# Performance work log

Measured on AMD Instinct MI355X. Metric: run time of the kernel, lower is better.

Reference implementation:

```python
import jax, jax.numpy as jnp
import numpy as np

N_NODES = 100000
N_EDGES = 1600000
STATE_DIM = 128
HIDDEN_DIM = 128
ACTION_DIM = 16


def gcn_conv(x, edge_index, W, b, n_nodes):
    """PyG-style GCNConv: add self-loops, symmetric normalization, x@W then aggregate."""
    xw = x @ W  # [N, H]
    loops = jnp.arange(n_nodes, dtype=edge_index.dtype)
    src = jnp.concatenate([edge_index[0], loops])  # [E+N]
    dst = jnp.concatenate([edge_index[1], loops])
    ones = jnp.ones(src.shape[0], dtype=xw.dtype)
    deg = jax.ops.segment_sum(ones, dst, num_segments=n_nodes)  # degree of target nodes
    dinv = jnp.where(deg > 0, jax.lax.rsqrt(deg), 0.0)
    norm = dinv[src] * dinv[dst]  # [E+N]
    msg = xw[src] * norm[:, None]  # gather + scale (irregular access)
    out = jax.ops.segment_sum(msg, dst, num_segments=n_nodes)  # scatter-aggregate
    return out + b


def setup_inputs() -> dict:
    key = jax.random.key(0)
    ks = jax.random.split(key, 12)
    def lin(k, fan_in, shape):
        bound = 1.0 / np.sqrt(fan_in)
        return jax.random.uniform(k, shape, jnp.float32, -bound, bound)
    return {
        "x": jax.random.normal(ks[0], (N_NODES, STATE_DIM), jnp.float32),
        "edge_index": jax.random.randint(ks[1], (2, N_EDGES), 0, N_NODES, jnp.int64),
        "action": jax.random.normal(ks[2], (N_NODES, ACTION_DIM), jnp.float32),
        "gcn1_w": lin(ks[3], STATE_DIM, (STATE_DIM, HIDDEN_DIM)),
        "gcn1_b": lin(ks[4], STATE_DIM, (HIDDEN_DIM,)),
        "gcn2_w": lin(ks[5], HIDDEN_DIM, (HIDDEN_DIM, HIDDEN_DIM)),
        "gcn2_b": lin(ks[6], HIDDEN_DIM, (HIDDEN_DIM,)),
        "fc1_w": lin(ks[7], HIDDEN_DIM + ACTION_DIM, (HIDDEN_DIM + ACTION_DIM, HIDDEN_DIM)),
        "fc1_b": lin(ks[8], HIDDEN_DIM + ACTION_DIM, (HIDDEN_DIM,)),
        "fc2_w": lin(ks[9], HIDDEN_DIM, (HIDDEN_DIM, 1)),
        "fc2_b": lin(ks[10], HIDDEN_DIM, (1,)),
    }


def reference(x, edge_index, action, gcn1_w, gcn1_b, gcn2_w, gcn2_b, fc1_w, fc1_b, fc2_w, fc2_b):
    n = x.shape[0]
    h = jax.nn.relu(gcn_conv(x, edge_index, gcn1_w, gcn1_b, n))
    h = jax.nn.relu(gcn_conv(h, edge_index, gcn2_w, gcn2_b, n))
    h = jnp.concatenate([h, action], axis=-1)  # [N, H+A]
    h = jax.nn.relu(h @ fc1_w + fc1_b)
    q = h @ fc2_w + fc2_b  # [N, 1]
    return q.squeeze(-1)
```

## Files before the change

### kernel.cpp

```cpp
#include <hip/hip_runtime.h>
#include <hip/hip_bf16.h>

typedef unsigned short u16;
typedef unsigned int   u32;
typedef __attribute__((ext_vector_type(8))) short bf16x8;
typedef __attribute__((ext_vector_type(4))) float f32x4;

constexpr int NN = 100000;
constexpr int NE = 1600000;
constexpr int D  = 128;
constexpr size_t WS_NEED = 58909184;

constexpr int NBUCK = 196;
constexpr int NBLKA = 256;
constexpr int EPB   = 6272;
constexpr int CAPA  = 80;

__device__ __forceinline__ float bf2f(u16 u){ union{u32 i;float f;}v; v.i=((u32)u)<<16; return v.f; }
__device__ __forceinline__ float2 bfp(u32 u){ union{u32 i;float f;}a,b; a.i=u<<16; b.i=u&0xffff0000u; return make_float2(a.f,b.f); }
__device__ __forceinline__ u16 f2bf(float f){ union{float f;u32 i;}v; v.f=f; u32 r=v.i + 0x7fffu + ((v.i>>16)&1u); return (u16)(r>>16); }
__device__ __forceinline__ u32 pk2(float a, float b){ return (u32)f2bf(a) | ((u32)f2bf(b)<<16); }

__global__ void detect_kernel(const u32* __restrict__ xw, const int* __restrict__ ei,
                              int* __restrict__ flagf, int* __restrict__ flage){
  __shared__ int shf[256];
  __shared__ int she[256];
  int t = threadIdx.x;
  int cnt = 0;
  for(int i = 0; i < 16; i++){
    u32 w = xw[(t*16 + i) * 256];
    int e = (int)((w >> 7) & 0xFFu);
    cnt += (e >= 64 && e <= 160) ? 1 : 0;
  }
  int nz = 0;
  for(int i = 0; i < 8; i++){
    int k = t*8 + i;
    long long w = 1 + ((long long)k * (2LL*NE - 2)) / 2048;
    nz += (ei[(int)(w | 1)] != 0) ? 1 : 0;
  }
  shf[t] = cnt; she[t] = nz;
  __syncthreads();
  for(int off=128; off>0; off>>=1){
    if(t<off){ shf[t]+=shf[t+off]; she[t]+=she[t+off]; }
    __syncthreads();
  }
  if(t==0){ flagf[0] = (shf[0] < 3000) ? 1 : 0; flage[0] = (she[0] == 0) ? 1 : 0; }
}

__global__ void prep_kernel(const void* __restrict__ w1, const void* __restrict__ w2,
    const void* __restrict__ fw1, const void* __restrict__ b1, const void* __restrict__ b2,
    const void* __restrict__ fb1, const void* __restrict__ fw2, const void* __restrict__ fb2,
    const int* __restrict__ flagf,
    u16* __restrict__ WT1, u16* __restrict__ WT2, u16* __restrict__ WTF, float* __restrict__ BF)
{
  const int ff = flagf[0];
  int i = blockIdx.x*256 + threadIdx.x;
  auto cv = [&](const void* p, int idx)->float{
    return ff ? ((const float*)p)[idx] : bf2f(((const u16*)p)[idx]);
  };
  if(i < 16384){
    int k = i >> 7, d = i & 127;
    WT1[d*128 + k] = f2bf(cv(w1, i));
  }else if(i < 32768){
    int j = i - 16384; int k = j >> 7, d = j & 127;
    WT2[d*128 + k] = f2bf(cv(w2, j));
  }else if(i < 51200){
    int j = i - 32768; int k = j >> 7, d = j & 127;
    WTF[d*144 + k] = f2bf(cv(fw1, j));
  }else if(i < 51713){
    int j = i - 51200;
    if(j < 128)       BF[j]   = cv(b1, j);
    else if(j < 256)  BF[j]   = cv(b2, j-128);
    else if(j < 384)  BF[j]   = cv(fb1, j-256);
    else if(j < 512)  BF[j]   = cv(fw2, j-384);
    else              BF[512] = cv(fb2, 0);
  }
}

__global__ void fill1_kernel(u16* __restrict__ out, int n){
  int i = blockIdx.x*blockDim.x + threadIdx.x;
  if(i < n) out[i] = 0x3F80;
}

__global__ __launch_bounds__(256) void passA_kernel(
    const int* __restrict__ ei, const int* __restrict__ flage,
    u32* __restrict__ ebuf, u32* __restrict__ counts)
{
  __shared__ u32 hist[NBUCK];
  int t = threadIdx.x;
  for(int b = t; b < NBUCK; b += 256) hist[b] = 0;
  __syncthreads();
  const int f = flage[0];
  const int eb = blockIdx.x * EPB;
  const u32 cbase = blockIdx.x * NBUCK;
  for(int i = t; i < EPB; i += 256){
    int e = eb + i;
    if(e >= NE) break;
    int s = f ? ei[2*e]      : ei[e];
    int d = f ? ei[2*(NE+e)] : ei[NE+e];
    if((u32)s >= (u32)NN || (u32)d >= (u32)NN) continue;
    int b = d >> 9;
    u32 rank = atomicAdd(&hist[b], 1u);
    if(rank < CAPA) ebuf[(size_t)(cbase + b)*CAPA + rank] = (u32)s | ((u32)(d & 511) << 17);
  }
  __syncthreads();
  for(int b = t; b < NBUCK; b += 256){
    u32 c = hist[b];
    counts[cbase + b] = (c < CAPA) ? c : CAPA;
  }
}

__global__ void scan196_kernel(const u32* __restrict__ counts, int* __restrict__ bases){
  __shared__ int sh[NBUCK];
  int t = threadIdx.x;
  if(t < NBUCK){
    int tot = 0;
    for(int c = 0; c < NBLKA; c++) tot += counts[c*NBUCK + t];
    sh[t] = tot;
  }
  __syncthreads();
  if(t == 0){
    int acc = 0;
    for(int b = 0; b < NBUCK; b++){ int v = sh[b]; sh[b] = acc; acc += v; }
  }
  __syncthreads();
  if(t < NBUCK) bases[t] = sh[t];
}

__global__ __launch_bounds__(512) void passB_kernel(
    const u32* __restrict__ ebuf, const u32* __restrict__ counts, const int* __restrict__ bases,
    int* __restrict__ deg, int* __restrict__ off, float* __restrict__ dinv,
    int* __restrict__ srcs)
{
  __shared__ int cnt[512];
  __shared__ int nodeoff[512];
  __shared__ int pos[512];
  __shared__ int choff[NBLKA + 1];
  const int t = threadIdx.x;
  const int b = blockIdx.x;
  const int v0 = b << 9;

  cnt[t] = 0;
  __syncthreads();

  if(t < NBLKA) choff[t] = (int)counts[t*NBUCK + b];
  __syncthreads();
  if(t == 0){
    int acc = 0;
    for(int c = 0; c < NBLKA; c++){ int v = choff[c]; choff[c] = acc; acc += v; }
    choff[NBLKA] = acc;
  }
  __syncthreads();
  const int T = choff[NBLKA];

  for(int i = t; i < T; i += 512){
    int lo = 0, hi = NBLKA - 1;
    #pragma unroll
    for(int s = 0; s < 8; s++){
      int mid = (lo + hi) >> 1;
      if(choff[mid + 1] <= i) lo = mid + 1; else hi = mid;
    }
    u32 rec = ebuf[(size_t)(lo*NBUCK + b)*CAPA + (i - choff[lo])];
    atomicAdd(&cnt[rec >> 17], 1);
  }
  __syncthreads();

  int myc = cnt[t];
  nodeoff[t] = myc;
  __syncthreads();
  for(int o = 1; o < 512; o <<= 1){
    int a = (t >= o) ? nodeoff[t - o] : 0;
    __syncthreads();
    nodeoff[t] += a;
    __syncthreads();
  }
  int excl = nodeoff[t] - myc;
  __syncthreads();
  nodeoff[t] = excl;
  pos[t] = 0;
  __syncthreads();

  const int gb = bases[b];

  for(int i = t; i < T; i += 512){
    int lo = 0, hi = NBLKA - 1;
    #pragma unroll
    for(int s = 0; s < 8; s++){
      int mid = (lo + hi) >> 1;
      if(choff[mid + 1] <= i) lo = mid + 1; else hi = mid;
    }
    u32 rec = ebuf[(size_t)(lo*NBUCK + b)*CAPA + (i - choff[lo])];
    int ld = rec >> 17;
    int r = atomicAdd(&pos[ld], 1);
    srcs[gb + nodeoff[ld] + r] = (int)(rec & 0x1FFFFu);
  }

  int v = v0 + t;
  if(v < NN){
    deg[v] = myc;
    off[v] = gb + excl;
    dinv[v] = rsqrtf((float)(myc + 1));
  }
}

template<int K, bool FUSE_Q, bool RAW1, bool RAW2>
__global__ __launch_bounds__(256) void gemm_mfma(
    const void* __restrict__ A1, const void* __restrict__ A2,
    const u16* __restrict__ WT, const float* __restrict__ biasf,
    const float* __restrict__ qwf, const float* __restrict__ qbf,
    const int* __restrict__ flagf, void* __restrict__ out, int n)
{
  constexpr int KT = ((K + 31)/32)*32;
  constexpr int KP = KT + 8;
  __shared__ u16 Ws[128*KP];
  __shared__ u16 As[64*KP];
  const int tid = threadIdx.x;
  const int nb  = blockIdx.x * 64;
  const int ff  = flagf[0];

  constexpr int CPT = KT/8;
  for(int i = tid; i < 128*CPT; i += 256){
    int row = i / CPT, col = (i % CPT) * 8;
    uint4 v = make_uint4(0,0,0,0);
    if(col < K) v = *(const uint4*)(WT + row*K + col);
    *(uint4*)(Ws + row*KP + col) = v;
  }
  for(int i = tid; i < 64*CPT; i += 256){
    int row = i / CPT, col = (i % CPT) * 8;
    int gr = nb + row; if(gr >= n) gr = n-1;
    uint4 v = make_uint4(0,0,0,0);
    if(col < 128){
      if(!RAW1 || !ff){
        v = *(const uint4*)((const u16*)A1 + (size_t)gr*128 + col);
      }else{
        const float* af = (const float*)A1 + (size_t)gr*128 + col;
        float4 p0 = *(const float4*)(af);
        float4 p1 = *(const float4*)(af + 4);
        v.x = pk2(p0.x,p0.y); v.y = pk2(p0.z,p0.w);
        v.z = pk2(p1.x,p1.y); v.w = pk2(p1.z,p1.w);
      }
    }else if(col < K){
      if(!RAW2 || !ff){
        v = *(const uint4*)((const u16*)A2 + (size_t)gr*16 + (col - 128));
      }else{
        const float* af = (const float*)A2 + (size_t)gr*16 + (col - 128);
        float4 p0 = *(const float4*)(af);
        float4 p1 = *(const float4*)(af + 4);
        v.x = pk2(p0.x,p0.y); v.y = pk2(p0.z,p0.w);
        v.z = pk2(p1.x,p1.y); v.w = pk2(p1.z,p1.w);
      }
    }
    *(uint4*)(As + row*KP + col) = v;
  }
  __syncthreads();

  const int wave = tid >> 6;
  const int lane = tid & 63;
  const int quad = lane >> 4;
  const int lm   = lane & 15;

  const u16* Ab = As + (wave*16 + lm)*KP;
  const u16* Bb = Ws + lm*KP;

  f32x4 acc[8];
  #pragma unroll
  for(int t=0;t<8;t++) acc[t] = (f32x4){0.f,0.f,0.f,0.f};

  #pragma unroll
  for(int ki = 0; ki < KT/32; ki++){
    int kk = ki*32 + quad*8;
    bf16x8 a = *(const bf16x8*)(Ab + kk);
    #pragma unroll
    for(int t=0;t<8;t++){
      bf16x8 b = *(const bf16x8*)(Bb + t*16*KP + kk);
      acc[t] = __builtin_amdgcn_mfma_f32_16x16x32_bf16(a, b, acc[t], 0, 0, 0);
    }
  }

  const int node0 = nb + wave*16 + quad*4;
  if(!FUSE_Q){
    #pragma unroll
    for(int t=0;t<8;t++){
      #pragma unroll
      for(int r=0;r<4;r++){
        int gr = node0 + r;
        if(gr < n) ((u16*)out)[(size_t)gr*D + t*16 + lm] = f2bf(acc[t][r]);
      }
    }
  }else{
    float qp[4] = {0.f,0.f,0.f,0.f};
    #pragma unroll
    for(int t=0;t<8;t++){
      float bvt = biasf[t*16 + lm];
      float qwt = qwf[t*16 + lm];
      #pragma unroll
      for(int r=0;r<4;r++){
        float h = fmaxf(acc[t][r] + bvt, 0.f);
        qp[r] += h * qwt;
      }
    }
    #pragma unroll
    for(int r=0;r<4;r++){
      #pragma unroll
      for(int o=1; o<16; o<<=1) qp[r] += __shfl_xor(qp[r], o, 16);
    }
    if(lm == 0){
      float qb = qbf[0];
      #pragma unroll
      for(int r=0;r<4;r++){
        int gr = node0 + r;
        if(gr < n){
          float q = qp[r] + qb;
          if(ff) ((float*)out)[gr] = q;
          else   ((u16*)out)[gr]  = f2bf(q);
        }
      }
    }
  }
}

__global__ __launch_bounds__(256) void gather_kernel(
    const int* __restrict__ off, const int* __restrict__ deg,
    const int* __restrict__ srcs, const float* __restrict__ dinv,
    const u16* __restrict__ xw, const float* __restrict__ biasf,
    u16* __restrict__ h)
{
  int node = blockIdx.x*8 + (threadIdx.x >> 5);
  int lane = threadIdx.x & 31;
  if(node >= NN) return;
  int j0 = off[node];
  int j1 = j0 + deg[node];

  float a0=0.f, a1=0.f, a2=0.f, a3=0.f;
  const size_t lo = 4*lane;
  int j = j0;
  for(; j+4 <= j1; j += 4){
    int s0=srcs[j], s1=srcs[j+1], s2=srcs[j+2], s3=srcs[j+3];
    if((u32)s0>=(u32)NN) s0=node; if((u32)s1>=(u32)NN) s1=node;
    if((u32)s2>=(u32)NN) s2=node; if((u32)s3>=(u32)NN) s3=node;
    float w0=dinv[s0], w1=dinv[s1], w2=dinv[s2], w3=dinv[s3];
    uint2 p0 = *(const uint2*)(xw + (size_t)s0*D + lo);
    uint2 p1 = *(const uint2*)(xw + (size_t)s1*D + lo);
    uint2 p2 = *(const uint2*)(xw + (size_t)s2*D + lo);
    uint2 p3 = *(const uint2*)(xw + (size_t)s3*D + lo);
    float2 f0a=bfp(p0.x), f0b=bfp(p0.y);
    float2 f1a=bfp(p1.x), f1b=bfp(p1.y);
    float2 f2a=bfp(p2.x), f2b=bfp(p2.y);
    float2 f3a=bfp(p3.x), f3b=bfp(p3.y);
    a0 += w0*f0a.x + w1*f1a.x + w2*f2a.x + w3*f3a.x;
    a1 += w0*f0a.y + w1*f1a.y + w2*f2a.y + w3*f3a.y;
    a2 += w0*f0b.x + w1*f1b.x + w2*f2b.x + w3*f3b.x;
    a3 += w0*f0b.y + w1*f1b.y + w2*f2b.y + w3*f3b.y;
  }
  for(; j < j1; j++){
    int s = srcs[j];
    if((u32)s >= (u32)NN) continue;
    float w = dinv[s];
    uint2 p = *(const uint2*)(xw + (size_t)s*D + lo);
    float2 fa=bfp(p.x), fb=bfp(p.y);
    a0 += w*fa.x; a1 += w*fa.y; a2 += w*fb.x; a3 += w*fb.y;
  }

  float dv = dinv[node];
  float dv2 = dv*dv;
  uint2 ps = *(const uint2*)(xw + (size_t)node*D + lo);
  float2 sa=bfp(ps.x), sb=bfp(ps.y);
  float4 bf4 = *(const float4*)(biasf + lo);
  float o0 = fmaxf(dv*a0 + dv2*sa.x + bf4.x, 0.f);
  float o1 = fmaxf(dv*a1 + dv2*sa.y + bf4.y, 0.f);
  float o2 = fmaxf(dv*a2 + dv2*sb.x + bf4.z, 0.f);
  float o3 = fmaxf(dv*a3 + dv2*sb.y + bf4.w, 0.f);
  uint2 pkd; pkd.x = pk2(o0,o1); pkd.y = pk2(o2,o3);
  *(uint2*)(h + (size_t)node*D + lo) = pkd;
}

extern "C" void kernel_launch(void* const* d_in, const int* in_sizes, int n_in,
                              void* d_out, int out_size, void* d_ws, size_t ws_size,
                              hipStream_t stream)
{
  bool meta_ok = (n_in >= 11) && (in_sizes[0] == NN*D) && (in_sizes[1] == 2*NE)
              && (in_sizes[2] == NN*16) && (out_size == NN);
  if(!meta_ok){
    fill1_kernel<<<(NN+255)/256, 256, 0, stream>>>((u16*)d_out, NN);
    return;
  }
  if(ws_size < WS_NEED) return;

  const void* x      = d_in[0];
  const int*  ei     = (const int*)d_in[1];
  const void* action = d_in[2];
  const void* w1     = d_in[3];
  const void* b1     = d_in[4];
  const void* w2     = d_in[5];
  const void* b2     = d_in[6];
  const void* fw1    = d_in[7];
  const void* fb1    = d_in[8];
  const void* fw2    = d_in[9];
  const void* fb2    = d_in[10];

  char* ws = (char*)d_ws;
  int*   DEG    = (int*)(ws + 0);
  int*   OFF    = (int*)(ws + 400128);
  float* DINV   = (float*)(ws + 800256);
  int*   FLAGE  = (int*)(ws + 1204480);
  int*   FLAGF  = (int*)(ws + 1204544);
  u16*   WT1    = (u16*)(ws + 1204608);
  u16*   WT2    = (u16*)(ws + 1237376);
  u16*   WTF    = (u16*)(ws + 1270144);
  float* BF     = (float*)(ws + 1307008);
  int*   SRCS   = (int*)(ws + 1309184);
  u16*   F0     = (u16*)(ws + 7709184);
  u16*   F1     = (u16*)(ws + 33309184);
  u32*   EBUF   = (u32*)(ws + 33309184);
  u32*   COUNTS = (u32*)(ws + 49365504);
  int*   BASES  = (int*)(ws + 49566208);

  detect_kernel<<<1, 256, 0, stream>>>((const u32*)x, ei, FLAGF, FLAGE);

  passA_kernel<<<NBLKA, 256, 0, stream>>>(ei, FLAGE, EBUF, COUNTS);
  scan196_kernel<<<1, 256, 0, stream>>>(COUNTS, BASES);
  passB_kernel<<<NBUCK, 512, 0, stream>>>(EBUF, COUNTS, BASES, DEG, OFF, DINV, SRCS);

  prep_kernel<<<203, 256, 0, stream>>>(w1, w2, fw1, b1, b2, fb1, fw2, fb2, FLAGF,
                                       WT1, WT2, WTF, BF);

  gemm_mfma<128,false,true,false><<<(NN+63)/64, 256, 0, stream>>>(x, nullptr, WT1, nullptr, nullptr, nullptr, FLAGF, F0, NN);
  gather_kernel<<<(NN+7)/8, 256, 0, stream>>>(OFF, DEG, SRCS, DINV, F0, BF, F1);

  gemm_mfma<128,false,false,false><<<(NN+63)/64, 256, 0, stream>>>(F1, nullptr, WT2, nullptr, nullptr, nullptr, FLAGF, F0, NN);
  gather_kernel<<<(NN+7)/8, 256, 0, stream>>>(OFF, DEG, SRCS, DINV, F0, BF+128, F1);

  gemm_mfma<144,true,false,true><<<(NN+63)/64, 256, 0, stream>>>(F1, action, WTF, BF+256, BF+384, BF+512, FLAGF, d_out, NN);
}
```

Before: 369.8 us.

## Fuse neighbor gather into following GEMM kernels, removing intermediate round-trips

The gather-aggregate step is moved into the GEMM kernel prologue. Each 256-thread block gathers 64 nodes' aggregated features directly into shared memory and then runs the MFMA GEMM, so the aggregated hidden features no longer make a round trip through global memory and two launches disappear. The gather inner loop is also unrolled to 8 edges so more loads are in flight. The trade-off is lower gather parallelism per block (8 groups each handling 8 nodes sequentially) and a larger shared-memory footprint during the gather, which may reduce the latency hiding that the standalone gather kernel had.

```diff
diff --git a/kernel.cpp b/kernel.cpp
--- a/kernel.cpp
+++ b/kernel.cpp
@@ -203,12 +203,124 @@
   }
 }
 
-template<int K, bool FUSE_Q, bool RAW1, bool RAW2>
+__device__ __forceinline__ void gather_node(
+    const int* __restrict__ off, const int* __restrict__ deg,
+    const int* __restrict__ srcs, const float* __restrict__ dinv,
+    const u16* __restrict__ xw, const float* __restrict__ biasf,
+    int node, int lane, u32& w0, u32& w1)
+{
+  int j0 = off[node];
+  int j1 = j0 + deg[node];
+  float a0=0.f, a1=0.f, a2=0.f, a3=0.f;
+  const size_t lo = 4*lane;
+  int j = j0;
+  for(; j+8 <= j1; j += 8){
+    int s[8]; float w[8]; uint2 p[8];
+    #pragma unroll
+    for(int u=0;u<8;u++){ int sv = srcs[j+u]; s[u] = ((u32)sv < (u32)NN) ? sv : node; }
+    #pragma unroll
+    for(int u=0;u<8;u++) w[u] = dinv[s[u]];
+    #pragma unroll
+    for(int u=0;u<8;u++) p[u] = *(const uint2*)(xw + (size_t)s[u]*D + lo);
+    #pragma unroll
+    for(int u=0;u<8;u++){
+      float2 fa=bfp(p[u].x), fb=bfp(p[u].y);
+      a0 += w[u]*fa.x; a1 += w[u]*fa.y; a2 += w[u]*fb.x; a3 += w[u]*fb.y;
+    }
+  }
+  for(; j < j1; j++){
+    int sv = srcs[j];
+    int s = ((u32)sv < (u32)NN) ? sv : node;
+    float w = dinv[s];
+    uint2 p = *(const uint2*)(xw + (size_t)s*D + lo);
+    float2 fa=bfp(p.x), fb=bfp(p.y);
+    a0 += w*fa.x; a1 += w*fa.y; a2 += w*fb.x; a3 += w*fb.y;
+  }
+  float dv = dinv[node];
+  float dv2 = dv*dv;
+  uint2 ps = *(const uint2*)(xw + (size_t)node*D + lo);
+  float2 sa=bfp(ps.x), sb=bfp(ps.y);
+  float4 bf4 = *(const float4*)(biasf + lo);
+  float o0 = fmaxf(dv*a0 + dv2*sa.x + bf4.x, 0.f);
+  float o1 = fmaxf(dv*a1 + dv2*sa.y + bf4.y, 0.f);
+  float o2 = fmaxf(dv*a2 + dv2*sb.x + bf4.z, 0.f);
+  float o3 = fmaxf(dv*a3 + dv2*sb.y + bf4.w, 0.f);
+  w0 = pk2(o0,o1); w1 = pk2(o2,o3);
+}
+
+template<bool RAW1>
 __global__ __launch_bounds__(256) void gemm_mfma(
-    const void* __restrict__ A1, const void* __restrict__ A2,
-    const u16* __restrict__ WT, const float* __restrict__ biasf,
-    const float* __restrict__ qwf, const float* __restrict__ qbf,
-    const int* __restrict__ flagf, void* __restrict__ out, int n)
+    const void* __restrict__ A1, const u16* __restrict__ WT,
+    const int* __restrict__ flagf, u16* __restrict__ out, int n)
+{
+  constexpr int KP = 128 + 8;
+  __shared__ u16 Ws[128*KP];
+  __shared__ u16 As[64*KP];
+  const int tid = threadIdx.x;
+  const int nb  = blockIdx.x * 64;
+  const int ff  = flagf[0];
+
+  for(int i = tid; i < 128*16; i += 256){
+    int row = i / 16, col = (i % 16) * 8;
+    *(uint4*)(Ws + row*KP + col) = *(const uint4*)(WT + row*128 + col);
+  }
+  for(int i = tid; i < 64*16; i += 256){
+    int row = i / 16, col = (i % 16) * 8;
+    int gr = nb + row; if(gr >= n) gr = n-1;
+    uint4 v;
+    if(!RAW1 || !ff){
+      v = *(const uint4*)((const u16*)A1 + (size_t)gr*128 + col);
+    }else{
+      const float* af = (const float*)A1 + (size_t)gr*128 + col;
+      float4 p0 = *(const float4*)(af);
+      float4 p1 = *(const float4*)(af + 4);
+      v.x = pk2(p0.x,p0.y); v.y = pk2(p0.z,p0.w);
+      v.z = pk2(p1.x,p1.y); v.w = pk2(p1.z,p1.w);
+    }
+    *(uint4*)(As + row*KP + col) = v;
+  }
+  __syncthreads();
+
+  const int wave = tid >> 6;
+  const int lane = tid & 63;
+  const int quad = lane >> 4;
+  const int lm   = lane & 15;
+  const u16* Ab = As + (wave*16 + lm)*KP;
+  const u16* Bb = Ws + lm*KP;
+
+  f32x4 acc[8];
+  #pragma unroll
+  for(int t=0;t<8;t++) acc[t] = (f32x4){0.f,0.f,0.f,0.f};
+  #pragma unroll
+  for(int ki = 0; ki < 4; ki++){
+    int kk = ki*32 + quad*8;
+    bf16x8 a = *(const bf16x8*)(Ab + kk);
+    #pragma unroll
+    for(int t=0;t<8;t++){
+      bf16x8 b = *(const bf16x8*)(Bb + t*16*KP + kk);
+      acc[t] = __builtin_amdgcn_mfma_f32_16x16x32_bf16(a, b, acc[t], 0, 0, 0);
+    }
+  }
+  const int node0 = nb + wave*16 + quad*4;
+  #pragma unroll
+  for(int t=0;t<8;t++){
+    #pragma unroll
+    for(int r=0;r<4;r++){
+      int gr = node0 + r;
+      if(gr < n) out[(size_t)gr*D + t*16 + lm] = f2bf(acc[t][r]);
+    }
+  }
+}
+
+template<int K, bool FUSE_Q, bool RAW2>
+__global__ __launch_bounds__(256) void gather_gemm(
+    const u16* __restrict__ xw, const void* __restrict__ A2,
+    const u16* __restrict__ WT, const float* __restrict__ biasg,
+    const float* __restrict__ biasf, const float* __restrict__ qwf,
+    const float* __restrict__ qbf, const int* __restrict__ flagf,
+    const int* __restrict__ off, const int* __restrict__ deg,
+    const int* __restrict__ srcs, const float* __restrict__ dinv,
+    void* __restrict__ out, int n)
 {
   constexpr int KT = ((K + 31)/32)*32;
   constexpr int KP = KT + 8;
@@ -225,32 +337,37 @@
     if(col < K) v = *(const uint4*)(WT + row*K + col);
     *(uint4*)(Ws + row*KP + col) = v;
   }
-  for(int i = tid; i < 64*CPT; i += 256){
-    int row = i / CPT, col = (i % CPT) * 8;
-    int gr = nb + row; if(gr >= n) gr = n-1;
-    uint4 v = make_uint4(0,0,0,0);
-    if(col < 128){
-      if(!RAW1 || !ff){
-        v = *(const uint4*)((const u16*)A1 + (size_t)gr*128 + col);
-      }else{
-        const float* af = (const float*)A1 + (size_t)gr*128 + col;
-        float4 p0 = *(const float4*)(af);
-        float4 p1 = *(const float4*)(af + 4);
-        v.x = pk2(p0.x,p0.y); v.y = pk2(p0.z,p0.w);
-        v.z = pk2(p1.x,p1.y); v.w = pk2(p1.z,p1.w);
+  if(KT > 128){
+    constexpr int C2 = (KT - 128)/8;
+    for(int i = tid; i < 64*C2; i += 256){
+      int row = i / C2, col = 128 + (i % C2) * 8;
+      int gr = nb + row; if(gr >= n) gr = n-1;
+      uint4 v = make_uint4(0,0,0,0);
+      if(col < K){
+        if(!RAW2 || !ff){
+          v = *(const uint4*)((const u16*)A2 + (size_t)gr*16 + (col - 128));
+        }else{
+          const float* af = (const float*)A2 + (size_t)gr*16 + (col - 128);
+          float4 p0 = *(const float4*)(af);
+          float4 p1 = *(const float4*)(af + 4);
+          v.x = pk2(p0.x,p0.y); v.y = pk2(p0.z,p0.w);
+          v.z = pk2(p1.x,p1.y); v.w = pk2(p1.z,p1.w);
+        }
       }
-    }else if(col < K){
-      if(!RAW2 || !ff){
-        v = *(const uint4*)((const u16*)A2 + (size_t)gr*16 + (col - 128));
-      }else{
-        const float* af = (const float*)A2 + (size_t)gr*16 + (col - 128);
-        float4 p0 = *(const float4*)(af);
-        float4 p1 = *(const float4*)(af + 4);
-        v.x = pk2(p0.x,p0.y); v.y = pk2(p0.z,p0.w);
-        v.z = pk2(p1.x,p1.y); v.w = pk2(p1.z,p1.w);
-      }
-    }
-    *(uint4*)(As + row*KP + col) = v;
+      *(uint4*)(As + row*KP + col) = v;
+    }
+  }
+  {
+    const int g = tid >> 5;
+    const int lane = tid & 31;
+    for(int i = 0; i < 8; i++){
+      int row = g*8 + i;
+      int node = nb + row; if(node >= n) node = n-1;
+      u32 w0, w1;
+      gather_node(off, deg, srcs, dinv, xw, biasg, node, lane, w0, w1);
+      uint2 pk; pk.x = w0; pk.y = w1;
+      *(uint2*)(As + row*KP + 4*lane) = pk;
+    }
   }
   __syncthreads();
 
@@ -258,14 +375,12 @@
   const int lane = tid & 63;
   const int quad = lane >> 4;
   const int lm   = lane & 15;
-
   const u16* Ab = As + (wave*16 + lm)*KP;
   const u16* Bb = Ws + lm*KP;
 
   f32x4 acc[8];
   #pragma unroll
   for(int t=0;t<8;t++) acc[t] = (f32x4){0.f,0.f,0.f,0.f};
-
   #pragma unroll
   for(int ki = 0; ki < KT/32; ki++){
     int kk = ki*32 + quad*8;
@@ -317,61 +432,6 @@
       }
     }
   }
-}
-
-__global__ __launch_bounds__(256) void gather_kernel(
-    const int* __restrict__ off, const int* __restrict__ deg,
-    const int* __restrict__ srcs, const float* __restrict__ dinv,
-    const u16* __restrict__ xw, const float* __restrict__ biasf,
-    u16* __restrict__ h)
-{
-  int node = blockIdx.x*8 + (threadIdx.x >> 5);
-  int lane = threadIdx.x & 31;
-  if(node >= NN) return;
-  int j0 = off[node];
-  int j1 = j0 + deg[node];
-
-  float a0=0.f, a1=0.f, a2=0.f, a3=0.f;
-  const size_t lo = 4*lane;
-  int j = j0;
-  for(; j+4 <= j1; j += 4){
-    int s0=srcs[j], s1=srcs[j+1], s2=srcs[j+2], s3=srcs[j+3];
-    if((u32)s0>=(u32)NN) s0=node; if((u32)s1>=(u32)NN) s1=node;
-    if((u32)s2>=(u32)NN) s2=node; if((u32)s3>=(u32)NN) s3=node;
-    float w0=dinv[s0], w1=dinv[s1], w2=dinv[s2], w3=dinv[s3];
-    uint2 p0 = *(const uint2*)(xw + (size_t)s0*D + lo);
-    uint2 p1 = *(const uint2*)(xw + (size_t)s1*D + lo);
-    uint2 p2 = *(const uint2*)(xw + (size_t)s2*D + lo);
-    uint2 p3 = *(const uint2*)(xw + (size_t)s3*D + lo);
-    float2 f0a=bfp(p0.x), f0b=bfp(p0.y);
-    float2 f1a=bfp(p1.x), f1b=bfp(p1.y);
-    float2 f2a=bfp(p2.x), f2b=bfp(p2.y);
-    float2 f3a=bfp(p3.x), f3b=bfp(p3.y);
-    a0 += w0*f0a.x + w1*f1a.x + w2*f2a.x + w3*f3a.x;
-    a1 += w0*f0a.y + w1*f1a.y + w2*f2a.y + w3*f3a.y;
-    a2 += w0*f0b.x + w1*f1b.x + w2*f2b.x + w3*f3b.x;
-    a3 += w0*f0b.y + w1*f1b.y + w2*f2b.y + w3*f3b.y;
-  }
-  for(; j < j1; j++){
-    int s = srcs[j];
-    if((u32)s >= (u32)NN) continue;
-    float w = dinv[s];
-    uint2 p = *(const uint2*)(xw + (size_t)s*D + lo);
-    float2 fa=bfp(p.x), fb=bfp(p.y);
-    a0 += w*fa.x; a1 += w*fa.y; a2 += w*fb.x; a3 += w*fb.y;
-  }
-
-  float dv = dinv[node];
-  float dv2 = dv*dv;
-  uint2 ps = *(const uint2*)(xw + (size_t)node*D + lo);
-  float2 sa=bfp(ps.x), sb=bfp(ps.y);
-  float4 bf4 = *(const float4*)(biasf + lo);
-  float o0 = fmaxf(dv*a0 + dv2*sa.x + bf4.x, 0.f);
-  float o1 = fmaxf(dv*a1 + dv2*sa.y + bf4.y, 0.f);
-  float o2 = fmaxf(dv*a2 + dv2*sb.x + bf4.z, 0.f);
-  float o3 = fmaxf(dv*a3 + dv2*sb.y + bf4.w, 0.f);
-  uint2 pkd; pkd.x = pk2(o0,o1); pkd.y = pk2(o2,o3);
-  *(uint2*)(h + (size_t)node*D + lo) = pkd;
 }
 
 extern "C" void kernel_launch(void* const* d_in, const int* in_sizes, int n_in,
@@ -424,11 +484,13 @@
   prep_kernel<<<203, 256, 0, stream>>>(w1, w2, fw1, b1, b2, fb1, fw2, fb2, FLAGF,
                                        WT1, WT2, WTF, BF);
 
-  gemm_mfma<128,false,true,false><<<(NN+63)/64, 256, 0, stream>>>(x, nullptr, WT1, nullptr, nullptr, nullptr, FLAGF, F0, NN);
-  gather_kernel<<<(NN+7)/8, 256, 0, stream>>>(OFF, DEG, SRCS, DINV, F0, BF, F1);
-
-  gemm_mfma<128,false,false,false><<<(NN+63)/64, 256, 0, stream>>>(F1, nullptr, WT2, nullptr, nullptr, nullptr, FLAGF, F0, NN);
-  gather_kernel<<<(NN+7)/8, 256, 0, stream>>>(OFF, DEG, SRCS, DINV, F0, BF+128, F1);
-
-  gemm_mfma<144,true,false,true><<<(NN+63)/64, 256, 0, stream>>>(F1, action, WTF, BF+256, BF+384, BF+512, FLAGF, d_out, NN);
-}
+  gemm_mfma<true><<<(NN+63)/64, 256, 0, stream>>>(x, WT1, FLAGF, F0, NN);
+
+  gather_gemm<128,false,false><<<(NN+63)/64, 256, 0, stream>>>(
+      F0, nullptr, WT2, BF, nullptr, nullptr, nullptr, FLAGF,
+      OFF, DEG, SRCS, DINV, F1, NN);
+
+  gather_gemm<144,true,true><<<(NN+63)/64, 256, 0, stream>>>(
+      F1, action, WTF, BF+128, BF+256, BF+384, BF+512, FLAGF,
+      OFF, DEG, SRCS, DINV, d_out, NN);
+}
```

After: 505.8 us. 1.37x slower.
